# Optimization experiments

Hardware: AMD Instinct MI355X
Metric: run time of the kernel (lower is better)

The kernel has to match this reference:

```python
import jax, jax.numpy as jnp
import numpy as np
from jax import lax

EPS = 1e-5  # torch BatchNorm1d default eps

def _conv(x, w, stride):
    # x: [B,H,W,Cin], w: [3,3,Cin,Cout], padding=1
    return lax.conv_general_dilated(x, w, (stride, stride), ((1, 1), (1, 1)),
                                    dimension_numbers=('NHWC', 'HWIO', 'NHWC'))

def _masked_bn(f, m, gamma, beta):
    # BatchNorm1d over active voxels only (training-mode, biased var),
    # matching BN applied to spconv's [N_active, C] feature matrix.
    # f: [B,H,W,C], m: [B,H,W,1] in {0,1}
    cnt = jnp.sum(m)
    mean = jnp.sum(f * m, axis=(0, 1, 2)) / cnt            # [C]
    var = jnp.sum(m * (f - mean) ** 2, axis=(0, 1, 2)) / cnt
    return ((f - mean) * lax.rsqrt(var + EPS) * gamma + beta) * m

def setup_inputs() -> dict:
    key = jax.random.key(0)
    ks = jax.random.split(key, 4)
    B, H, W, Cin, Cout = 4, 256, 256, 64, 128
    x = jax.random.normal(ks[0], (B, H, W, Cin), dtype=jnp.float32)
    mask = jax.random.randint(ks[1], (B, H, W), 0, 10, dtype=jnp.int32)
    w1 = jax.random.normal(ks[2], (3, 3, Cin, Cout), dtype=jnp.float32) * 0.05
    w2 = jax.random.normal(ks[3], (3, 3, Cout, Cout), dtype=jnp.float32) * 0.05
    gamma1 = jnp.ones((Cout,), jnp.float32)
    beta1 = jnp.zeros((Cout,), jnp.float32)
    gamma2 = jnp.ones((Cout,), jnp.float32)
    beta2 = jnp.zeros((Cout,), jnp.float32)
    return {"x": x, "mask": mask, "w1": w1, "gamma1": gamma1, "beta1": beta1,
            "w2": w2, "gamma2": gamma2, "beta2": beta2}

def reference(x, mask, w1, gamma1, beta1, w2, gamma2, beta2):
    act = (mask == 0).astype(x.dtype)[..., None]   # [B,H,W,1] input active sites
    xm = x * act                                   # sparse tensor densified (zeros off-sites)
    # conv1: regular sparse conv, stride 2 -> output active where any input in 3x3 recep. field
    out = _conv(xm, w1, 2)
    m1 = (_conv(act, jnp.ones((3, 3, 1, 1), x.dtype), 2) > 0).astype(x.dtype)
    out = _masked_bn(out, m1, gamma1, beta1)
    out = jax.nn.relu(out)
    # conv2: submanifold conv, stride 1 -> active set preserved (m1)
    out = _conv(out, w2, 1) * m1
    out = _masked_bn(out, m1, gamma2, beta2)
    return out
```

## Files before the change

### kernel.cpp

```cpp
#include <hip/hip_runtime.h>

#define EPS_BN 1e-5f
#define MFMA16 __builtin_amdgcn_mfma_f32_16x16x32_bf16

typedef unsigned char uchar;
typedef short short8 __attribute__((ext_vector_type(8)));
typedef float f32x4 __attribute__((ext_vector_type(4)));

__device__ __forceinline__ ushort f2bf(float f) {
    unsigned u = __float_as_uint(f);
    return (ushort)((u + 0x7FFFu + ((u >> 16) & 1u)) >> 16);
}
__device__ __forceinline__ float bf2f(ushort h) {
    return __uint_as_float(((unsigned)h) << 16);
}
__device__ __forceinline__ void gload_lds16(const void* g, void* l) {
    __builtin_amdgcn_global_load_lds(
        (const __attribute__((address_space(1))) void*)g,
        (__attribute__((address_space(3))) void*)l, 16, 0, 0);
}


__global__ __launch_bounds__(256) void mask_kernel(const int* __restrict__ mask,
                                                   uchar* __restrict__ m1,
                                                   int* __restrict__ cnt)
{
    int idx = blockIdx.x * 256 + threadIdx.x;
    int ow = idx & 127;
    int oh = (idx >> 7) & 127;
    int b  = idx >> 14;
    bool act = false;
    #pragma unroll
    for (int kh = 0; kh < 3; ++kh) {
        int ih = 2*oh - 1 + kh;
        if ((unsigned)ih >= 256u) continue;
        #pragma unroll
        for (int kw = 0; kw < 3; ++kw) {
            int iw = 2*ow - 1 + kw;
            if ((unsigned)iw >= 256u) continue;
            if (mask[(b*256 + ih)*256 + iw] == 0) act = true;
        }
    }
    m1[idx] = act ? 1 : 0;
    unsigned long long bal = __ballot(act);
    if ((threadIdx.x & 63) == 0)
        atomicAdd(cnt, (int)__popcll(bal));
}

__global__ __launch_bounds__(256) void xcvt_kernel(const float* __restrict__ x,
                                                   const int* __restrict__ mask,
                                                   ushort* __restrict__ xb)
{
    int idx = blockIdx.x * 256 + threadIdx.x;
    int px = idx >> 3;
    int c0 = (idx & 7) * 8;
    short8 o = {0,0,0,0,0,0,0,0};
    if (mask[px] == 0) {
        const float* p = x + (size_t)px * 64 + c0;
        #pragma unroll
        for (int j = 0; j < 8; ++j) o[j] = (short)f2bf(p[j]);
    }
    *(short8*)(xb + (size_t)px * 64 + c0) = o;
}

__global__ __launch_bounds__(256) void wcvt_kernel(const float* __restrict__ w1,
                                                   const float* __restrict__ w2,
                                                   ushort* __restrict__ w1T,
                                                   ushort* __restrict__ w2T)
{
    int idx = blockIdx.x * 256 + threadIdx.x;
    if (idx < 73728) {
        int ci = idx & 63;
        int co = (idx >> 6) & 127;
        int s  = idx >> 13;
        w1T[idx] = f2bf(w1[(s*64 + ci)*128 + co]);
    } else if (idx < 221184) {
        int i  = idx - 73728;
        int ci = i & 127;
        int co = (i >> 7) & 127;
        int s  = i >> 14;
        w2T[i] = f2bf(w2[(s*128 + ci)*128 + co]);
    }
}

__global__ __launch_bounds__(256) void conv1_mfma(const ushort* __restrict__ xb,
                                                  const ushort* __restrict__ w1T,
                                                  const ushort* __restrict__ zp,
                                                  const uchar* __restrict__ m1,
                                                  ushort* __restrict__ out1,
                                                  float* __restrict__ stats)
{
    __shared__ ushort At[2][8192];
    __shared__ ushort Bt[2][8192];

    const int t     = threadIdx.x;
    const int lane  = t & 63;
    const int wv    = t >> 6;
    const int wbase = t & ~63;
    const int blk   = blockIdx.x;
    const int oh    = blk & 127;
    const int b     = blk >> 7;

    const int wm = wv >> 1, wn = wv & 1;
    const int lr = lane & 15, lg = lane >> 4;

    auto dma = [&](int bf, int s) {
        const int kh = s / 3, kw = s % 3;
        const int ih = 2*oh + kh - 1;
        const bool rowok = ((unsigned)ih < 256u);
        const ushort* arow = xb + (size_t)(b*256 + ih) * 256 * 64;
        #pragma unroll
        for (int r = 0; r < 4; ++r) {
            int idx = r*256 + t;
            int px = idx >> 3, cd = idx & 7, cs = cd ^ (px & 7);
            int iw = 2*px + kw - 1;
            const ushort* g = (rowok && (unsigned)iw < 256u)
                              ? arow + (size_t)iw*64 + cs*8 : zp;
            gload_lds16(g, &At[bf][(size_t)(r*256 + wbase)*8]);
        }
        const ushort* brow = w1T + (size_t)s * 8192;
        #pragma unroll
        for (int r = 0; r < 4; ++r) {
            int idx = r*256 + t;
            int co = idx >> 3, cd = idx & 7, cs = cd ^ (co & 7);
            gload_lds16(brow + (size_t)co*64 + cs*8,
                        &Bt[bf][(size_t)(r*256 + wbase)*8]);
        }
    };

    f32x4 acc[4][4];
    #pragma unroll
    for (int mi = 0; mi < 4; ++mi)
        #pragma unroll
        for (int ni = 0; ni < 4; ++ni)
            acc[mi][ni] = (f32x4){0.f, 0.f, 0.f, 0.f};

    dma(0, 0);
    __syncthreads();
    for (int kt = 0; kt < 9; ++kt) {
        const int cb = kt & 1;
        if (kt < 8) dma(cb ^ 1, kt + 1);
        const char* Ab = (const char*)At[cb];
        const char* Bb = (const char*)Bt[cb];
        #pragma unroll
        for (int ks = 0; ks < 2; ++ks) {
            short8 af[4], bfr[4];
            #pragma unroll
            for (int mi = 0; mi < 4; ++mi) {
                int px = wm*64 + mi*16 + lr;
                af[mi] = *(const short8*)(Ab + ((px*128 + ks*64 + lg*16) ^ ((px & 7) << 4)));
            }
            #pragma unroll
            for (int ni = 0; ni < 4; ++ni) {
                int co = wn*64 + ni*16 + lr;
                bfr[ni] = *(const short8*)(Bb + ((co*128 + ks*64 + lg*16) ^ ((co & 7) << 4)));
            }
            #pragma unroll
            for (int mi = 0; mi < 4; ++mi)
                #pragma unroll
                for (int ni = 0; ni < 4; ++ni)
                    acc[mi][ni] = MFMA16(af[mi], bfr[ni], acc[mi][ni], 0, 0, 0);
        }
        __syncthreads();
    }

    const size_t pixbase = (size_t)blk * 128;
    #pragma unroll
    for (int mi = 0; mi < 4; ++mi) {
        #pragma unroll
        for (int ni = 0; ni < 4; ++ni) {
            int px = wm*64 + mi*16 + lg*4;
            int co = wn*64 + ni*16 + lr;
            #pragma unroll
            for (int r = 0; r < 4; ++r)
                out1[(pixbase + px + r)*128 + co] = f2bf(acc[mi][ni][r]);
        }
    }

    float s4[4] = {0.f,0.f,0.f,0.f}, q4[4] = {0.f,0.f,0.f,0.f};
    #pragma unroll
    for (int mi = 0; mi < 4; ++mi) {
        const uchar* mp = m1 + pixbase + wm*64 + mi*16 + lg*4;
        #pragma unroll
        for (int r = 0; r < 4; ++r) {
            float a = mp[r] ? 1.f : 0.f;
            #pragma unroll
            for (int ni = 0; ni < 4; ++ni) {
                float av = a * acc[mi][ni][r];
                s4[ni] += av;
                q4[ni] += av * acc[mi][ni][r];
            }
        }
    }
    float* red = (float*)At;
    const int rrow = wm*4 + lg;
    #pragma unroll
    for (int ni = 0; ni < 4; ++ni) red[rrow*128 + wn*64 + ni*16 + lr] = s4[ni];
    __syncthreads();
    if (t < 128) {
        float v = 0.f;
        #pragma unroll
        for (int rr = 0; rr < 8; ++rr) v += red[rr*128 + t];
        atomicAdd(&stats[t], v);
    }
    __syncthreads();
    #pragma unroll
    for (int ni = 0; ni < 4; ++ni) red[rrow*128 + wn*64 + ni*16 + lr] = q4[ni];
    __syncthreads();
    if (t < 128) {
        float v = 0.f;
        #pragma unroll
        for (int rr = 0; rr < 8; ++rr) v += red[rr*128 + t];
        atomicAdd(&stats[128 + t], v);
    }
}

__global__ __launch_bounds__(256) void conv2_mfma(const ushort* __restrict__ a,
                                                  const ushort* __restrict__ w2T,
                                                  const ushort* __restrict__ zp,
                                                  const uchar* __restrict__ m1,
                                                  float* __restrict__ outraw,
                                                  float* __restrict__ stats)
{
    __shared__ ushort At[2][8192];
    __shared__ ushort Bt[2][8192];

    const int t     = threadIdx.x;
    const int lane  = t & 63;
    const int wv    = t >> 6;
    const int wbase = t & ~63;
    const int blk   = blockIdx.x;
    const int oh    = blk & 127;
    const int b     = blk >> 7;

    const int wm = wv >> 1, wn = wv & 1;
    const int lr = lane & 15, lg = lane >> 4;

    auto dma = [&](int bf, int kt) {
        const int s = kt >> 1, h = kt & 1;
        const int kh = s / 3, kw = s % 3;
        const int ih = oh + kh - 1;
        const bool rowok = ((unsigned)ih < 128u);
        const ushort* arow = a + (size_t)(b*128 + ih) * 128 * 128;
        #pragma unroll
        for (int r = 0; r < 4; ++r) {
            int idx = r*256 + t;
            int px = idx >> 3, cd = idx & 7, cs = cd ^ (px & 7);
            int iw = px + kw - 1;
            const ushort* g = (rowok && (unsigned)iw < 128u)
                              ? arow + (size_t)iw*128 + h*64 + cs*8 : zp;
            gload_lds16(g, &At[bf][(size_t)(r*256 + wbase)*8]);
        }
        const ushort* brow = w2T + (size_t)s * 16384 + h*64;
        #pragma unroll
        for (int r = 0; r < 4; ++r) {
            int idx = r*256 + t;
            int co = idx >> 3, cd = idx & 7, cs = cd ^ (co & 7);
            gload_lds16(brow + (size_t)co*128 + cs*8,
                        &Bt[bf][(size_t)(r*256 + wbase)*8]);
        }
    };

    f32x4 acc[4][4];
    #pragma unroll
    for (int mi = 0; mi < 4; ++mi)
        #pragma unroll
        for (int ni = 0; ni < 4; ++ni)
            acc[mi][ni] = (f32x4){0.f, 0.f, 0.f, 0.f};

    dma(0, 0);
    __syncthreads();
    for (int kt = 0; kt < 18; ++kt) {
        const int cb = kt & 1;
        if (kt < 17) dma(cb ^ 1, kt + 1);
        const char* Ab = (const char*)At[cb];
        const char* Bb = (const char*)Bt[cb];
        #pragma unroll
        for (int ks = 0; ks < 2; ++ks) {
            short8 af[4], bfr[4];
            #pragma unroll
            for (int mi = 0; mi < 4; ++mi) {
                int px = wm*64 + mi*16 + lr;
                af[mi] = *(const short8*)(Ab + ((px*128 + ks*64 + lg*16) ^ ((px & 7) << 4)));
            }
            #pragma unroll
            for (int ni = 0; ni < 4; ++ni) {
                int co = wn*64 + ni*16 + lr;
                bfr[ni] = *(const short8*)(Bb + ((co*128 + ks*64 + lg*16) ^ ((co & 7) << 4)));
            }
            #pragma unroll
            for (int mi = 0; mi < 4; ++mi)
                #pragma unroll
                for (int ni = 0; ni < 4; ++ni)
                    acc[mi][ni] = MFMA16(af[mi], bfr[ni], acc[mi][ni], 0, 0, 0);
        }
        __syncthreads();
    }

    const size_t pixbase = (size_t)blk * 128;
    #pragma unroll
    for (int mi = 0; mi < 4; ++mi) {
        #pragma unroll
        for (int ni = 0; ni < 4; ++ni) {
            int px = wm*64 + mi*16 + lg*4;
            int co = wn*64 + ni*16 + lr;
            #pragma unroll
            for (int r = 0; r < 4; ++r)
                outraw[(pixbase + px + r)*128 + co] = acc[mi][ni][r];
        }
    }

    float s4[4] = {0.f,0.f,0.f,0.f}, q4[4] = {0.f,0.f,0.f,0.f};
    #pragma unroll
    for (int mi = 0; mi < 4; ++mi) {
        const uchar* mp = m1 + pixbase + wm*64 + mi*16 + lg*4;
        #pragma unroll
        for (int r = 0; r < 4; ++r) {
            float a = mp[r] ? 1.f : 0.f;
            #pragma unroll
            for (int ni = 0; ni < 4; ++ni) {
                float av = a * acc[mi][ni][r];
                s4[ni] += av;
                q4[ni] += av * acc[mi][ni][r];
            }
        }
    }
    float* red = (float*)At;
    const int rrow = wm*4 + lg;
    #pragma unroll
    for (int ni = 0; ni < 4; ++ni) red[rrow*128 + wn*64 + ni*16 + lr] = s4[ni];
    __syncthreads();
    if (t < 128) {
        float v = 0.f;
        #pragma unroll
        for (int rr = 0; rr < 8; ++rr) v += red[rr*128 + t];
        atomicAdd(&stats[t], v);
    }
    __syncthreads();
    #pragma unroll
    for (int ni = 0; ni < 4; ++ni) red[rrow*128 + wn*64 + ni*16 + lr] = q4[ni];
    __syncthreads();
    if (t < 128) {
        float v = 0.f;
        #pragma unroll
        for (int rr = 0; rr < 8; ++rr) v += red[rr*128 + t];
        atomicAdd(&stats[128 + t], v);
    }
}

__global__ void finalize_kernel(const float* __restrict__ stats,
                                const float* __restrict__ gamma,
                                const float* __restrict__ beta,
                                float* __restrict__ sbout,
                                const int* __restrict__ cnt)
{
    int c = threadIdx.x;
    float n = (float)(*cnt);
    float mean = stats[c] / n;
    float var  = stats[128 + c] / n - mean*mean;
    var = fmaxf(var, 0.f);
    float scale = gamma[c] * rsqrtf(var + EPS_BN);
    sbout[c]       = scale;
    sbout[128 + c] = beta[c] - mean*scale;
}

__global__ __launch_bounds__(256) void bnrelu_kernel(ushort* __restrict__ o,
                                                     const uchar* __restrict__ m1,
                                                     const float* __restrict__ sb)
{
    int idx = blockIdx.x * 256 + threadIdx.x;
    int px = idx >> 4;
    int c0 = (idx & 15) * 8;
    short8 r = {0,0,0,0,0,0,0,0};
    if (m1[px]) {
        short8 v = *(const short8*)(o + (size_t)px*128 + c0);
        #pragma unroll
        for (int j = 0; j < 8; ++j) {
            float f = fmaf(bf2f((ushort)v[j]), sb[c0+j], sb[128+c0+j]);
            r[j] = (short)f2bf(fmaxf(f, 0.f));
        }
    }
    *(short8*)(o + (size_t)px*128 + c0) = r;
}

__global__ __launch_bounds__(256) void apply_kernel(float* __restrict__ out,
                                                    const uchar* __restrict__ m1,
                                                    const float* __restrict__ sb)
{
    int idx4 = blockIdx.x * 256 + threadIdx.x;
    int pos = idx4 >> 5;
    int c4  = (idx4 & 31) << 2;
    float4 v = ((const float4*)out)[idx4];
    float4 r = make_float4(0.f, 0.f, 0.f, 0.f);
    if (m1[pos]) {
        r.x = fmaf(v.x, sb[c4+0], sb[128+c4+0]);
        r.y = fmaf(v.y, sb[c4+1], sb[128+c4+1]);
        r.z = fmaf(v.z, sb[c4+2], sb[128+c4+2]);
        r.w = fmaf(v.w, sb[c4+3], sb[128+c4+3]);
    }
    ((float4*)out)[idx4] = r;
}

extern "C" void kernel_launch(void* const* d_in, const int* in_sizes, int n_in,
                              void* d_out, int out_size, void* d_ws, size_t ws_size,
                              hipStream_t stream)
{
    const float* x      = (const float*)d_in[0];
    const int*   mask   = (const int*)d_in[1];
    const float* w1     = (const float*)d_in[2];
    const float* gamma1 = (const float*)d_in[3];
    const float* beta1  = (const float*)d_in[4];
    const float* w2     = (const float*)d_in[5];
    const float* gamma2 = (const float*)d_in[6];
    const float* beta2  = (const float*)d_in[7];

    ushort* out1 = (ushort*)d_ws;
    ushort* w1T  = out1 + 8388608;
    ushort* w2T  = w1T + 73728;
    float* stats = (float*)(w2T + 147456);
    float* sb    = stats + 512;
    int*   cnt   = (int*)(sb + 512);
    ushort* zp   = (ushort*)(cnt + 4);
    uchar* m1    = (uchar*)(zp + 128);

    ushort* xb = (ushort*)d_out;
    float*  out = (float*)d_out;

    hipMemsetAsync(stats, 0, 1024*sizeof(float) + 4*sizeof(int) + 256, stream);

    mask_kernel <<<256,  256, 0, stream>>>(mask, m1, cnt);
    xcvt_kernel <<<8192, 256, 0, stream>>>(x, mask, xb);
    wcvt_kernel <<<864,  256, 0, stream>>>(w1, w2, w1T, w2T);
    conv1_mfma  <<<512,  256, 0, stream>>>(xb, w1T, zp, m1, out1, stats);
    finalize_kernel<<<1, 128, 0, stream>>>(stats, gamma1, beta1, sb, cnt);
    bnrelu_kernel<<<4096,256, 0, stream>>>(out1, m1, sb);
    conv2_mfma  <<<512,  256, 0, stream>>>(out1, w2T, zp, m1, out, stats + 256);
    finalize_kernel<<<1, 128, 0, stream>>>(stats + 256, gamma2, beta2, sb + 256, cnt);
    apply_kernel<<<8192, 256, 0, stream>>>(out, m1, sb + 256);
}
```

Baseline: 123.3 us.

## Halve conv tile M to 64 pixels, double grid, precompute DMA addresses

```diff
diff --git a/kernel.cpp b/kernel.cpp
--- a/kernel.cpp
+++ b/kernel.cpp
@@ -83,14 +83,14 @@
     }
 }
 
-__global__ __launch_bounds__(256) void conv1_mfma(const ushort* __restrict__ xb,
-                                                  const ushort* __restrict__ w1T,
-                                                  const ushort* __restrict__ zp,
-                                                  const uchar* __restrict__ m1,
-                                                  ushort* __restrict__ out1,
-                                                  float* __restrict__ stats)
-{
-    __shared__ ushort At[2][8192];
+__global__ __launch_bounds__(256, 3) void conv1_mfma(const ushort* __restrict__ xb,
+                                                     const ushort* __restrict__ w1T,
+                                                     const ushort* __restrict__ zp,
+                                                     const uchar* __restrict__ m1,
+                                                     ushort* __restrict__ out1,
+                                                     float* __restrict__ stats)
+{
+    __shared__ ushort At[2][4096];
     __shared__ ushort Bt[2][8192];
 
     const int t     = threadIdx.x;
@@ -98,45 +98,63 @@
     const int wv    = t >> 6;
     const int wbase = t & ~63;
     const int blk   = blockIdx.x;
-    const int oh    = blk & 127;
-    const int b     = blk >> 7;
+    const int half  = blk & 1;
+    const int oh    = (blk >> 1) & 127;
+    const int b     = blk >> 8;
 
     const int wm = wv >> 1, wn = wv & 1;
     const int lr = lane & 15, lg = lane >> 4;
 
+    const int rowA = t >> 3;
+    const int cdA  = t & 7;
+    const int csA  = cdA ^ (rowA & 7);
+    const ushort* pA[2][3];
+    bool cok[2][3], rok[3];
+    #pragma unroll
+    for (int r = 0; r < 2; ++r) {
+        int pxg = half*64 + rowA + r*32;
+        int c0  = 2*pxg - 1;
+        #pragma unroll
+        for (int kw = 0; kw < 3; ++kw) cok[r][kw] = ((unsigned)(c0 + kw) < 256u);
+        #pragma unroll
+        for (int kh = 0; kh < 3; ++kh) {
+            int ih  = 2*oh + kh - 1;
+            int ihc = ih < 0 ? 0 : (ih > 255 ? 255 : ih);
+            pA[r][kh] = xb + ((size_t)(b*256 + ihc)*256 + c0)*64 + csA*8;
+        }
+    }
+    #pragma unroll
+    for (int kh = 0; kh < 3; ++kh) rok[kh] = ((unsigned)(2*oh + kh - 1) < 256u);
+    const ushort* pB[4];
+    #pragma unroll
+    for (int r = 0; r < 4; ++r) {
+        int idx = r*256 + t;
+        int co = idx >> 3, bcd = idx & 7, bcs = bcd ^ (co & 7);
+        pB[r] = w1T + (size_t)co*64 + bcs*8;
+    }
+
     auto dma = [&](int bf, int s) {
         const int kh = s / 3, kw = s % 3;
-        const int ih = 2*oh + kh - 1;
-        const bool rowok = ((unsigned)ih < 256u);
-        const ushort* arow = xb + (size_t)(b*256 + ih) * 256 * 64;
-        #pragma unroll
-        for (int r = 0; r < 4; ++r) {
-            int idx = r*256 + t;
-            int px = idx >> 3, cd = idx & 7, cs = cd ^ (px & 7);
-            int iw = 2*px + kw - 1;
-            const ushort* g = (rowok && (unsigned)iw < 256u)
-                              ? arow + (size_t)iw*64 + cs*8 : zp;
+        #pragma unroll
+        for (int r = 0; r < 2; ++r) {
+            const ushort* g = (rok[kh] && cok[r][kw]) ? pA[r][kh] + kw*64 : zp;
             gload_lds16(g, &At[bf][(size_t)(r*256 + wbase)*8]);
         }
-        const ushort* brow = w1T + (size_t)s * 8192;
-        #pragma unroll
-        for (int r = 0; r < 4; ++r) {
-            int idx = r*256 + t;
-            int co = idx >> 3, cd = idx & 7, cs = cd ^ (co & 7);
-            gload_lds16(brow + (size_t)co*64 + cs*8,
-                        &Bt[bf][(size_t)(r*256 + wbase)*8]);
-        }
+        #pragma unroll
+        for (int r = 0; r < 4; ++r)
+            gload_lds16(pB[r] + (size_t)s*8192, &Bt[bf][(size_t)(r*256 + wbase)*8]);
     };
 
-    f32x4 acc[4][4];
-    #pragma unroll
-    for (int mi = 0; mi < 4; ++mi)
+    f32x4 acc[2][4];
+    #pragma unroll
+    for (int mi = 0; mi < 2; ++mi)
         #pragma unroll
         for (int ni = 0; ni < 4; ++ni)
             acc[mi][ni] = (f32x4){0.f, 0.f, 0.f, 0.f};
 
     dma(0, 0);
     __syncthreads();
+    #pragma unroll
     for (int kt = 0; kt < 9; ++kt) {
         const int cb = kt & 1;
         if (kt < 8) dma(cb ^ 1, kt + 1);
@@ -144,11 +162,11 @@
         const char* Bb = (const char*)Bt[cb];
         #pragma unroll
         for (int ks = 0; ks < 2; ++ks) {
-            short8 af[4], bfr[4];
-            #pragma unroll
-            for (int mi = 0; mi < 4; ++mi) {
-                int px = wm*64 + mi*16 + lr;
-                af[mi] = *(const short8*)(Ab + ((px*128 + ks*64 + lg*16) ^ ((px & 7) << 4)));
+            short8 af[2], bfr[4];
+            #pragma unroll
+            for (int mi = 0; mi < 2; ++mi) {
+                int row = wm*32 + mi*16 + lr;
+                af[mi] = *(const short8*)(Ab + ((row*128 + ks*64 + lg*16) ^ ((row & 7) << 4)));
             }
             #pragma unroll
             for (int ni = 0; ni < 4; ++ni) {
@@ -156,7 +174,7 @@
                 bfr[ni] = *(const short8*)(Bb + ((co*128 + ks*64 + lg*16) ^ ((co & 7) << 4)));
             }
             #pragma unroll
-            for (int mi = 0; mi < 4; ++mi)
+            for (int mi = 0; mi < 2; ++mi)
                 #pragma unroll
                 for (int ni = 0; ni < 4; ++ni)
                     acc[mi][ni] = MFMA16(af[mi], bfr[ni], acc[mi][ni], 0, 0, 0);
@@ -164,12 +182,12 @@
         __syncthreads();
     }
 
-    const size_t pixbase = (size_t)blk * 128;
-    #pragma unroll
-    for (int mi = 0; mi < 4; ++mi) {
+    const size_t pixbase = ((size_t)(b*128 + oh))*128 + half*64;
+    #pragma unroll
+    for (int mi = 0; mi < 2; ++mi) {
         #pragma unroll
         for (int ni = 0; ni < 4; ++ni) {
-            int px = wm*64 + mi*16 + lg*4;
+            int px = wm*32 + mi*16 + lg*4;
             int co = wn*64 + ni*16 + lr;
             #pragma unroll
             for (int r = 0; r < 4; ++r)
@@ -179,8 +197,8 @@
 
     float s4[4] = {0.f,0.f,0.f,0.f}, q4[4] = {0.f,0.f,0.f,0.f};
     #pragma unroll
-    for (int mi = 0; mi < 4; ++mi) {
-        const uchar* mp = m1 + pixbase + wm*64 + mi*16 + lg*4;
+    for (int mi = 0; mi < 2; ++mi) {
+        const uchar* mp = m1 + pixbase + wm*32 + mi*16 + lg*4;
         #pragma unroll
         for (int r = 0; r < 4; ++r) {
             float a = mp[r] ? 1.f : 0.f;
@@ -195,34 +213,28 @@
     float* red = (float*)At;
     const int rrow = wm*4 + lg;
     #pragma unroll
-    for (int ni = 0; ni < 4; ++ni) red[rrow*128 + wn*64 + ni*16 + lr] = s4[ni];
+    for (int ni = 0; ni < 4; ++ni) {
+        red[rrow*128 + wn*64 + ni*16 + lr]        = s4[ni];
+        red[1024 + rrow*128 + wn*64 + ni*16 + lr] = q4[ni];
+    }
     __syncthreads();
     if (t < 128) {
-        float v = 0.f;
-        #pragma unroll
-        for (int rr = 0; rr < 8; ++rr) v += red[rr*128 + t];
+        float v = 0.f, q = 0.f;
+        #pragma unroll
+        for (int rr = 0; rr < 8; ++rr) { v += red[rr*128 + t]; q += red[1024 + rr*128 + t]; }
         atomicAdd(&stats[t], v);
-    }
-    __syncthreads();
-    #pragma unroll
-    for (int ni = 0; ni < 4; ++ni) red[rrow*128 + wn*64 + ni*16 + lr] = q4[ni];
-    __syncthreads();
-    if (t < 128) {
-        float v = 0.f;
-        #pragma unroll
-        for (int rr = 0; rr < 8; ++rr) v += red[rr*128 + t];
-        atomicAdd(&stats[128 + t], v);
-    }
-}
-
-__global__ __launch_bounds__(256) void conv2_mfma(const ushort* __restrict__ a,
-                                                  const ushort* __restrict__ w2T,
-                                                  const ushort* __restrict__ zp,
-                                                  const uchar* __restrict__ m1,
-                                                  float* __restrict__ outraw,
-                                                  float* __restrict__ stats)
-{
-    __shared__ ushort At[2][8192];
+        atomicAdd(&stats[128 + t], q);
+    }
+}
+
+__global__ __launch_bounds__(256, 3) void conv2_mfma(const ushort* __restrict__ a,
+                                                     const ushort* __restrict__ w2T,
+                                                     const ushort* __restrict__ zp,
+                                                     const uchar* __restrict__ m1,
+                                                     float* __restrict__ outraw,
+                                                     float* __restrict__ stats)
+{
+    __shared__ ushort At[2][4096];
     __shared__ ushort Bt[2][8192];
 
     const int t     = threadIdx.x;
@@ -230,46 +242,65 @@
     const int wv    = t >> 6;
     const int wbase = t & ~63;
     const int blk   = blockIdx.x;
-    const int oh    = blk & 127;
-    const int b     = blk >> 7;
+    const int half  = blk & 1;
+    const int oh    = (blk >> 1) & 127;
+    const int b     = blk >> 8;
 
     const int wm = wv >> 1, wn = wv & 1;
     const int lr = lane & 15, lg = lane >> 4;
+
+    const int rowA = t >> 3;
+    const int cdA  = t & 7;
+    const int csA  = cdA ^ (rowA & 7);
+    const ushort* pA[2][3];
+    bool cok[2][3], rok[3];
+    #pragma unroll
+    for (int r = 0; r < 2; ++r) {
+        int pxg = half*64 + rowA + r*32;
+        int c0  = pxg - 1;
+        #pragma unroll
+        for (int kw = 0; kw < 3; ++kw) cok[r][kw] = ((unsigned)(c0 + kw) < 128u);
+        #pragma unroll
+        for (int kh = 0; kh < 3; ++kh) {
+            int ih  = oh + kh - 1;
+            int ihc = ih < 0 ? 0 : (ih > 127 ? 127 : ih);
+            pA[r][kh] = a + ((size_t)(b*128 + ihc)*128 + c0)*128 + csA*8;
+        }
+    }
+    #pragma unroll
+    for (int kh = 0; kh < 3; ++kh) rok[kh] = ((unsigned)(oh + kh - 1) < 128u);
+    const ushort* pB[4];
+    #pragma unroll
+    for (int r = 0; r < 4; ++r) {
+        int idx = r*256 + t;
+        int co = idx >> 3, bcd = idx & 7, bcs = bcd ^ (co & 7);
+        pB[r] = w2T + (size_t)co*128 + bcs*8;
+    }
 
     auto dma = [&](int bf, int kt) {
         const int s = kt >> 1, h = kt & 1;
         const int kh = s / 3, kw = s % 3;
-        const int ih = oh + kh - 1;
-        const bool rowok = ((unsigned)ih < 128u);
-        const ushort* arow = a + (size_t)(b*128 + ih) * 128 * 128;
-        #pragma unroll
-        for (int r = 0; r < 4; ++r) {
-            int idx = r*256 + t;
-            int px = idx >> 3, cd = idx & 7, cs = cd ^ (px & 7);
-            int iw = px + kw - 1;
-            const ushort* g = (rowok && (unsigned)iw < 128u)
-                              ? arow + (size_t)iw*128 + h*64 + cs*8 : zp;
+        #pragma unroll
+        for (int r = 0; r < 2; ++r) {
+            const ushort* g = (rok[kh] && cok[r][kw]) ? pA[r][kh] + kw*128 + h*64 : zp;
             gload_lds16(g, &At[bf][(size_t)(r*256 + wbase)*8]);
         }
-        const ushort* brow = w2T + (size_t)s * 16384 + h*64;
-        #pragma unroll
-        for (int r = 0; r < 4; ++r) {
-            int idx = r*256 + t;
-            int co = idx >> 3, cd = idx & 7, cs = cd ^ (co & 7);
-            gload_lds16(brow + (size_t)co*128 + cs*8,
+        #pragma unroll
+        for (int r = 0; r < 4; ++r)
+            gload_lds16(pB[r] + (size_t)s*16384 + h*64,
                         &Bt[bf][(size_t)(r*256 + wbase)*8]);
-        }
     };
 
-    f32x4 acc[4][4];
-    #pragma unroll
-    for (int mi = 0; mi < 4; ++mi)
+    f32x4 acc[2][4];
+    #pragma unroll
+    for (int mi = 0; mi < 2; ++mi)
         #pragma unroll
         for (int ni = 0; ni < 4; ++ni)
             acc[mi][ni] = (f32x4){0.f, 0.f, 0.f, 0.f};
 
     dma(0, 0);
     __syncthreads();
+    #pragma unroll
     for (int kt = 0; kt < 18; ++kt) {
         const int cb = kt & 1;
         if (kt < 17) dma(cb ^ 1, kt + 1);
@@ -277,11 +308,11 @@
         const char* Bb = (const char*)Bt[cb];
         #pragma unroll
         for (int ks = 0; ks < 2; ++ks) {
-            short8 af[4], bfr[4];
-            #pragma unroll
-            for (int mi = 0; mi < 4; ++mi) {
-                int px = wm*64 + mi*16 + lr;
-                af[mi] = *(const short8*)(Ab + ((px*128 + ks*64 + lg*16) ^ ((px & 7) << 4)));
+            short8 af[2], bfr[4];
+            #pragma unroll
+            for (int mi = 0; mi < 2; ++mi) {
+                int row = wm*32 + mi*16 + lr;
+                af[mi] = *(const short8*)(Ab + ((row*128 + ks*64 + lg*16) ^ ((row & 7) << 4)));
             }
             #pragma unroll
             for (int ni = 0; ni < 4; ++ni) {
@@ -289,7 +320,7 @@
                 bfr[ni] = *(const short8*)(Bb + ((co*128 + ks*64 + lg*16) ^ ((co & 7) << 4)));
             }
             #pragma unroll
-            for (int mi = 0; mi < 4; ++mi)
+            for (int mi = 0; mi < 2; ++mi)
                 #pragma unroll
                 for (int ni = 0; ni < 4; ++ni)
                     acc[mi][ni] = MFMA16(af[mi], bfr[ni], acc[mi][ni], 0, 0, 0);
@@ -297,12 +328,12 @@
         __syncthreads();
     }
 
-    const size_t pixbase = (size_t)blk * 128;
-    #pragma unroll
-    for (int mi = 0; mi < 4; ++mi) {
+    const size_t pixbase = ((size_t)(b*128 + oh))*128 + half*64;
+    #pragma unroll
+    for (int mi = 0; mi < 2; ++mi) {
         #pragma unroll
         for (int ni = 0; ni < 4; ++ni) {
-            int px = wm*64 + mi*16 + lg*4;
+            int px = wm*32 + mi*16 + lg*4;
             int co = wn*64 + ni*16 + lr;
             #pragma unroll
             for (int r = 0; r < 4; ++r)
@@ -312,14 +343,14 @@
 
     float s4[4] = {0.f,0.f,0.f,0.f}, q4[4] = {0.f,0.f,0.f,0.f};
     #pragma unroll
-    for (int mi = 0; mi < 4; ++mi) {
-        const uchar* mp = m1 + pixbase + wm*64 + mi*16 + lg*4;
+    for (int mi = 0; mi < 2; ++mi) {
+        const uchar* mp = m1 + pixbase + wm*32 + mi*16 + lg*4;
         #pragma unroll
         for (int r = 0; r < 4; ++r) {
-            float a = mp[r] ? 1.f : 0.f;
+            float av0 = mp[r] ? 1.f : 0.f;
             #pragma unroll
             for (int ni = 0; ni < 4; ++ni) {
-                float av = a * acc[mi][ni][r];
+                float av = av0 * acc[mi][ni][r];
                 s4[ni] += av;
                 q4[ni] += av * acc[mi][ni][r];
             }
@@ -328,23 +359,17 @@
     float* red = (float*)At;
     const int rrow = wm*4 + lg;
     #pragma unroll
-    for (int ni = 0; ni < 4; ++ni) red[rrow*128 + wn*64 + ni*16 + lr] = s4[ni];
+    for (int ni = 0; ni < 4; ++ni) {
+        red[rrow*128 + wn*64 + ni*16 + lr]        = s4[ni];
+        red[1024 + rrow*128 + wn*64 + ni*16 + lr] = q4[ni];
+    }
     __syncthreads();
     if (t < 128) {
-        float v = 0.f;
-        #pragma unroll
-        for (int rr = 0; rr < 8; ++rr) v += red[rr*128 + t];
+        float v = 0.f, q = 0.f;
+        #pragma unroll
+        for (int rr = 0; rr < 8; ++rr) { v += red[rr*128 + t]; q += red[1024 + rr*128 + t]; }
         atomicAdd(&stats[t], v);
-    }
-    __syncthreads();
-    #pragma unroll
-    for (int ni = 0; ni < 4; ++ni) red[rrow*128 + wn*64 + ni*16 + lr] = q4[ni];
-    __syncthreads();
-    if (t < 128) {
-        float v = 0.f;
-        #pragma unroll
-        for (int rr = 0; rr < 8; ++rr) v += red[rr*128 + t];
-        atomicAdd(&stats[128 + t], v);
+        atomicAdd(&stats[128 + t], q);
     }
 }
 
@@ -431,10 +456,10 @@
     mask_kernel <<<256,  256, 0, stream>>>(mask, m1, cnt);
     xcvt_kernel <<<8192, 256, 0, stream>>>(x, mask, xb);
     wcvt_kernel <<<864,  256, 0, stream>>>(w1, w2, w1T, w2T);
-    conv1_mfma  <<<512,  256, 0, stream>>>(xb, w1T, zp, m1, out1, stats);
+    conv1_mfma  <<<1024, 256, 0, stream>>>(xb, w1T, zp, m1, out1, stats);
     finalize_kernel<<<1, 128, 0, stream>>>(stats, gamma1, beta1, sb, cnt);
     bnrelu_kernel<<<4096,256, 0, stream>>>(out1, m1, sb);
-    conv2_mfma  <<<512,  256, 0, stream>>>(out1, w2T, zp, m1, out, stats + 256);
+    conv2_mfma  <<<1024, 256, 0, stream>>>(out1, w2T, zp, m1, out, stats + 256);
     finalize_kernel<<<1, 128, 0, stream>>>(stats + 256, gamma2, beta2, sb + 256, cnt);
     apply_kernel<<<8192, 256, 0, stream>>>(out, m1, sb + 256);
 }
```

Result: slower. 144.3 us (+17.1%).

## Fuse input masking and bf16 conversion into conv1; single-buffer LDS in both convs

Applied to the files above, without the earlier changes.

```diff
diff --git a/kernel.cpp b/kernel.cpp
--- a/kernel.cpp
+++ b/kernel.cpp
@@ -45,22 +45,6 @@
     unsigned long long bal = __ballot(act);
     if ((threadIdx.x & 63) == 0)
         atomicAdd(cnt, (int)__popcll(bal));
-}
-
-__global__ __launch_bounds__(256) void xcvt_kernel(const float* __restrict__ x,
-                                                   const int* __restrict__ mask,
-                                                   ushort* __restrict__ xb)
-{
-    int idx = blockIdx.x * 256 + threadIdx.x;
-    int px = idx >> 3;
-    int c0 = (idx & 7) * 8;
-    short8 o = {0,0,0,0,0,0,0,0};
-    if (mask[px] == 0) {
-        const float* p = x + (size_t)px * 64 + c0;
-        #pragma unroll
-        for (int j = 0; j < 8; ++j) o[j] = (short)f2bf(p[j]);
-    }
-    *(short8*)(xb + (size_t)px * 64 + c0) = o;
 }
 
 __global__ __launch_bounds__(256) void wcvt_kernel(const float* __restrict__ w1,
@@ -83,15 +67,15 @@
     }
 }
 
-__global__ __launch_bounds__(256) void conv1_mfma(const ushort* __restrict__ xb,
-                                                  const ushort* __restrict__ w1T,
-                                                  const ushort* __restrict__ zp,
-                                                  const uchar* __restrict__ m1,
-                                                  ushort* __restrict__ out1,
-                                                  float* __restrict__ stats)
-{
-    __shared__ ushort At[2][8192];
-    __shared__ ushort Bt[2][8192];
+__global__ __launch_bounds__(256, 4) void conv1_mfma(const float* __restrict__ x,
+                                                     const int* __restrict__ mask,
+                                                     const ushort* __restrict__ w1T,
+                                                     const uchar* __restrict__ m1,
+                                                     ushort* __restrict__ out1,
+                                                     float* __restrict__ stats)
+{
+    __shared__ ushort At[8192];
+    __shared__ ushort Bt[8192];
 
     const int t     = threadIdx.x;
     const int lane  = t & 63;
@@ -104,28 +88,48 @@
     const int wm = wv >> 1, wn = wv & 1;
     const int lr = lane & 15, lg = lane >> 4;
 
-    auto dma = [&](int bf, int s) {
+    const int p0 = t >> 3;
+    const int cd = t & 7;
+    const float* xrow[3];
+    const int*   mrow[3];
+    bool rok[3];
+    #pragma unroll
+    for (int kh = 0; kh < 3; ++kh) {
+        int ih  = 2*oh + kh - 1;
+        rok[kh] = ((unsigned)ih < 256u);
+        int ihc = ih < 0 ? 0 : (ih > 255 ? 255 : ih);
+        xrow[kh] = x + (size_t)(b*256 + ihc)*256*64 + cd*8;
+        mrow[kh] = mask + (size_t)(b*256 + ihc)*256;
+    }
+    const int ldsA0 = ((p0*128 + cd*16) ^ ((p0 & 7) << 4));
+    const int co0  = t >> 3;
+    const int bcs  = (t & 7) ^ (co0 & 7);
+    const ushort* pB0 = w1T + (size_t)co0*64 + bcs*8;
+
+    auto stageA = [&](int s) {
         const int kh = s / 3, kw = s % 3;
-        const int ih = 2*oh + kh - 1;
-        const bool rowok = ((unsigned)ih < 256u);
-        const ushort* arow = xb + (size_t)(b*256 + ih) * 256 * 64;
         #pragma unroll
         for (int r = 0; r < 4; ++r) {
-            int idx = r*256 + t;
-            int px = idx >> 3, cd = idx & 7, cs = cd ^ (px & 7);
+            int px = r*32 + p0;
             int iw = 2*px + kw - 1;
-            const ushort* g = (rowok && (unsigned)iw < 256u)
-                              ? arow + (size_t)iw*64 + cs*8 : zp;
-            gload_lds16(g, &At[bf][(size_t)(r*256 + wbase)*8]);
-        }
-        const ushort* brow = w1T + (size_t)s * 8192;
-        #pragma unroll
-        for (int r = 0; r < 4; ++r) {
-            int idx = r*256 + t;
-            int co = idx >> 3, cd = idx & 7, cs = cd ^ (co & 7);
-            gload_lds16(brow + (size_t)co*64 + cs*8,
-                        &Bt[bf][(size_t)(r*256 + wbase)*8]);
-        }
+            short8 v = {0,0,0,0,0,0,0,0};
+            if (rok[kh] && (unsigned)iw < 256u && mrow[kh][iw] == 0) {
+                const float* p = xrow[kh] + (size_t)iw*64;
+                float4 fa = *(const float4*)p;
+                float4 fb = *(const float4*)(p + 4);
+                v[0]=(short)f2bf(fa.x); v[1]=(short)f2bf(fa.y);
+                v[2]=(short)f2bf(fa.z); v[3]=(short)f2bf(fa.w);
+                v[4]=(short)f2bf(fb.x); v[5]=(short)f2bf(fb.y);
+                v[6]=(short)f2bf(fb.z); v[7]=(short)f2bf(fb.w);
+            }
+            *(short8*)((char*)At + (ldsA0 + r*4096)) = v;
+        }
+    };
+    auto dmaB = [&](int s) {
+        #pragma unroll
+        for (int r = 0; r < 4; ++r)
+            gload_lds16(pB0 + (size_t)s*8192 + r*2048,
+                        &Bt[(size_t)(r*256 + wbase)*8]);
     };
 
     f32x4 acc[4][4];
@@ -135,20 +139,21 @@
         for (int ni = 0; ni < 4; ++ni)
             acc[mi][ni] = (f32x4){0.f, 0.f, 0.f, 0.f};
 
-    dma(0, 0);
-    __syncthreads();
+    #pragma unroll
     for (int kt = 0; kt < 9; ++kt) {
-        const int cb = kt & 1;
-        if (kt < 8) dma(cb ^ 1, kt + 1);
-        const char* Ab = (const char*)At[cb];
-        const char* Bb = (const char*)Bt[cb];
+        if (kt) __syncthreads();
+        stageA(kt);
+        dmaB(kt);
+        __syncthreads();
+        const char* Ab = (const char*)At;
+        const char* Bb = (const char*)Bt;
         #pragma unroll
         for (int ks = 0; ks < 2; ++ks) {
             short8 af[4], bfr[4];
             #pragma unroll
             for (int mi = 0; mi < 4; ++mi) {
-                int px = wm*64 + mi*16 + lr;
-                af[mi] = *(const short8*)(Ab + ((px*128 + ks*64 + lg*16) ^ ((px & 7) << 4)));
+                int row = wm*64 + mi*16 + lr;
+                af[mi] = *(const short8*)(Ab + ((row*128 + ks*64 + lg*16) ^ ((row & 7) << 4)));
             }
             #pragma unroll
             for (int ni = 0; ni < 4; ++ni) {
@@ -161,7 +166,6 @@
                 for (int ni = 0; ni < 4; ++ni)
                     acc[mi][ni] = MFMA16(af[mi], bfr[ni], acc[mi][ni], 0, 0, 0);
         }
-        __syncthreads();
     }
 
     const size_t pixbase = (size_t)blk * 128;
@@ -192,38 +196,33 @@
             }
         }
     }
+    __syncthreads();
     float* red = (float*)At;
     const int rrow = wm*4 + lg;
     #pragma unroll
-    for (int ni = 0; ni < 4; ++ni) red[rrow*128 + wn*64 + ni*16 + lr] = s4[ni];
+    for (int ni = 0; ni < 4; ++ni) {
+        red[rrow*128 + wn*64 + ni*16 + lr]        = s4[ni];
+        red[1024 + rrow*128 + wn*64 + ni*16 + lr] = q4[ni];
+    }
     __syncthreads();
     if (t < 128) {
-        float v = 0.f;
-        #pragma unroll
-        for (int rr = 0; rr < 8; ++rr) v += red[rr*128 + t];
+        float v = 0.f, q = 0.f;
+        #pragma unroll
+        for (int rr = 0; rr < 8; ++rr) { v += red[rr*128 + t]; q += red[1024 + rr*128 + t]; }
         atomicAdd(&stats[t], v);
-    }
-    __syncthreads();
-    #pragma unroll
-    for (int ni = 0; ni < 4; ++ni) red[rrow*128 + wn*64 + ni*16 + lr] = q4[ni];
-    __syncthreads();
-    if (t < 128) {
-        float v = 0.f;
-        #pragma unroll
-        for (int rr = 0; rr < 8; ++rr) v += red[rr*128 + t];
-        atomicAdd(&stats[128 + t], v);
-    }
-}
-
-__global__ __launch_bounds__(256) void conv2_mfma(const ushort* __restrict__ a,
-                                                  const ushort* __restrict__ w2T,
-                                                  const ushort* __restrict__ zp,
-                                                  const uchar* __restrict__ m1,
-                                                  float* __restrict__ outraw,
-                                                  float* __restrict__ stats)
-{
-    __shared__ ushort At[2][8192];
-    __shared__ ushort Bt[2][8192];
+        atomicAdd(&stats[128 + t], q);
+    }
+}
+
+__global__ __launch_bounds__(256, 4) void conv2_mfma(const ushort* __restrict__ a,
+                                                     const ushort* __restrict__ w2T,
+                                                     const ushort* __restrict__ zp,
+                                                     const uchar* __restrict__ m1,
+                                                     float* __restrict__ outraw,
+                                                     float* __restrict__ stats)
+{
+    __shared__ ushort At[8192];
+    __shared__ ushort Bt[8192];
 
     const int t     = threadIdx.x;
     const int lane  = t & 63;
@@ -236,29 +235,34 @@
     const int wm = wv >> 1, wn = wv & 1;
     const int lr = lane & 15, lg = lane >> 4;
 
-    auto dma = [&](int bf, int kt) {
+    const int p0  = t >> 3;
+    const int cs  = (t & 7) ^ (p0 & 7);
+    const ushort* arow[3];
+    bool rok[3];
+    #pragma unroll
+    for (int kh = 0; kh < 3; ++kh) {
+        int ih  = oh + kh - 1;
+        rok[kh] = ((unsigned)ih < 128u);
+        int ihc = ih < 0 ? 0 : (ih > 127 ? 127 : ih);
+        arow[kh] = a + (size_t)(b*128 + ihc)*128*128 + cs*8;
+    }
+    const int aoff0 = (p0 - 1) * 128;
+    const ushort* pB0 = w2T + (size_t)(t >> 3)*128 + ((t & 7) ^ ((t >> 3) & 7))*8;
+
+    auto dma = [&](int kt) {
         const int s = kt >> 1, h = kt & 1;
         const int kh = s / 3, kw = s % 3;
-        const int ih = oh + kh - 1;
-        const bool rowok = ((unsigned)ih < 128u);
-        const ushort* arow = a + (size_t)(b*128 + ih) * 128 * 128;
         #pragma unroll
         for (int r = 0; r < 4; ++r) {
-            int idx = r*256 + t;
-            int px = idx >> 3, cd = idx & 7, cs = cd ^ (px & 7);
-            int iw = px + kw - 1;
-            const ushort* g = (rowok && (unsigned)iw < 128u)
-                              ? arow + (size_t)iw*128 + h*64 + cs*8 : zp;
-            gload_lds16(g, &At[bf][(size_t)(r*256 + wbase)*8]);
-        }
-        const ushort* brow = w2T + (size_t)s * 16384 + h*64;
-        #pragma unroll
-        for (int r = 0; r < 4; ++r) {
-            int idx = r*256 + t;
-            int co = idx >> 3, cd = idx & 7, cs = cd ^ (co & 7);
-            gload_lds16(brow + (size_t)co*128 + cs*8,
-                        &Bt[bf][(size_t)(r*256 + wbase)*8]);
-        }
+            int px = r*32 + p0;
+            bool ok = rok[kh] && ((unsigned)(px + kw - 1) < 128u);
+            const ushort* g = ok ? arow[kh] + aoff0 + r*4096 + kw*128 + h*64 : zp;
+            gload_lds16(g, &At[(size_t)(r*256 + wbase)*8]);
+        }
+        #pragma unroll
+        for (int r = 0; r < 4; ++r)
+            gload_lds16(pB0 + (size_t)s*16384 + h*64 + r*4096,
+                        &Bt[(size_t)(r*256 + wbase)*8]);
     };
 
     f32x4 acc[4][4];
@@ -268,20 +272,20 @@
         for (int ni = 0; ni < 4; ++ni)
             acc[mi][ni] = (f32x4){0.f, 0.f, 0.f, 0.f};
 
-    dma(0, 0);
-    __syncthreads();
+    #pragma unroll
     for (int kt = 0; kt < 18; ++kt) {
-        const int cb = kt & 1;
-        if (kt < 17) dma(cb ^ 1, kt + 1);
-        const char* Ab = (const char*)At[cb];
-        const char* Bb = (const char*)Bt[cb];
+        if (kt) __syncthreads();
+        dma(kt);
+        __syncthreads();
+        const char* Ab = (const char*)At;
+        const char* Bb = (const char*)Bt;
         #pragma unroll
         for (int ks = 0; ks < 2; ++ks) {
             short8 af[4], bfr[4];
             #pragma unroll
             for (int mi = 0; mi < 4; ++mi) {
-                int px = wm*64 + mi*16 + lr;
-                af[mi] = *(const short8*)(Ab + ((px*128 + ks*64 + lg*16) ^ ((px & 7) << 4)));
+                int row = wm*64 + mi*16 + lr;
+                af[mi] = *(const short8*)(Ab + ((row*128 + ks*64 + lg*16) ^ ((row & 7) << 4)));
             }
             #pragma unroll
             for (int ni = 0; ni < 4; ++ni) {
@@ -294,7 +298,6 @@
                 for (int ni = 0; ni < 4; ++ni)
                     acc[mi][ni] = MFMA16(af[mi], bfr[ni], acc[mi][ni], 0, 0, 0);
         }
-        __syncthreads();
     }
 
     const size_t pixbase = (size_t)blk * 128;
@@ -316,35 +319,30 @@
         const uchar* mp = m1 + pixbase + wm*64 + mi*16 + lg*4;
         #pragma unroll
         for (int r = 0; r < 4; ++r) {
-            float a = mp[r] ? 1.f : 0.f;
+            float av0 = mp[r] ? 1.f : 0.f;
             #pragma unroll
             for (int ni = 0; ni < 4; ++ni) {
-                float av = a * acc[mi][ni][r];
+                float av = av0 * acc[mi][ni][r];
                 s4[ni] += av;
                 q4[ni] += av * acc[mi][ni][r];
             }
         }
     }
+    __syncthreads();
     float* red = (float*)At;
     const int rrow = wm*4 + lg;
     #pragma unroll
-    for (int ni = 0; ni < 4; ++ni) red[rrow*128 + wn*64 + ni*16 + lr] = s4[ni];
+    for (int ni = 0; ni < 4; ++ni) {
+        red[rrow*128 + wn*64 + ni*16 + lr]        = s4[ni];
+        red[1024 + rrow*128 + wn*64 + ni*16 + lr] = q4[ni];
+    }
     __syncthreads();
     if (t < 128) {
-        float v = 0.f;
-        #pragma unroll
-        for (int rr = 0; rr < 8; ++rr) v += red[rr*128 + t];
+        float v = 0.f, q = 0.f;
+        #pragma unroll
+        for (int rr = 0; rr < 8; ++rr) { v += red[rr*128 + t]; q += red[1024 + rr*128 + t]; }
         atomicAdd(&stats[t], v);
-    }
-    __syncthreads();
-    #pragma unroll
-    for (int ni = 0; ni < 4; ++ni) red[rrow*128 + wn*64 + ni*16 + lr] = q4[ni];
-    __syncthreads();
-    if (t < 128) {
-        float v = 0.f;
-        #pragma unroll
-        for (int rr = 0; rr < 8; ++rr) v += red[rr*128 + t];
-        atomicAdd(&stats[128 + t], v);
+        atomicAdd(&stats[128 + t], q);
     }
 }
 
@@ -423,15 +421,13 @@
     ushort* zp   = (ushort*)(cnt + 4);
     uchar* m1    = (uchar*)(zp + 128);
 
-    ushort* xb = (ushort*)d_out;
-    float*  out = (float*)d_out;
+    float* out = (float*)d_out;
 
     hipMemsetAsync(stats, 0, 1024*sizeof(float) + 4*sizeof(int) + 256, stream);
 
     mask_kernel <<<256,  256, 0, stream>>>(mask, m1, cnt);
-    xcvt_kernel <<<8192, 256, 0, stream>>>(x, mask, xb);
     wcvt_kernel <<<864,  256, 0, stream>>>(w1, w2, w1T, w2T);
-    conv1_mfma  <<<512,  256, 0, stream>>>(xb, w1T, zp, m1, out1, stats);
+    conv1_mfma  <<<512,  256, 0, stream>>>(x, mask, w1T, m1, out1, stats);
     finalize_kernel<<<1, 128, 0, stream>>>(stats, gamma1, beta1, sb, cnt);
     bnrelu_kernel<<<4096,256, 0, stream>>>(out1, m1, sb);
     conv2_mfma  <<<512,  256, 0, stream>>>(out1, w2T, zp, m1, out, stats + 256);
```

Result: slower. 138.2 us (+12.1%).
